# Optimization experiments

Measured on AMD Instinct MI355X. Metric: run time of the kernel, lower is better.

## Reference

```python
import jax, jax.numpy as jnp
import numpy as np

N_CELL, N_NET, N_GCELL = 50000, 10000, 20000
E = 100000
D = 32   # hidden_node = hidden_net = hidden_hanna = out_node = out_net
DP = 16  # hidden_pin = hidden_edge feats


def setup_inputs() -> dict:
    key = jax.random.key(0)
    ks = jax.random.split(key, 21)
    f = jax.random.normal
    ri = lambda k, n: jax.random.randint(k, (E,), 0, n, dtype=jnp.int32)
    return {
        'node_feat': f(ks[0], (N_CELL, D), jnp.float32),
        'net_feat': f(ks[1], (N_NET, D), jnp.float32),
        'pin_feat': f(ks[2], (E, DP), jnp.float32),
        'hanna_feat': f(ks[3], (N_GCELL, D), jnp.float32),
        'edge_feat': f(ks[4], (E, DP), jnp.float32),
        'pins_src': ri(ks[5], N_CELL), 'pins_dst': ri(ks[6], N_NET),
        'pinned_src': ri(ks[7], N_NET), 'pinned_dst': ri(ks[8], N_CELL),
        'connect_src': ri(ks[9], N_GCELL), 'connect_dst': ri(ks[10], N_GCELL),
        'pt_src': ri(ks[11], N_CELL), 'pt_dst': ri(ks[12], N_GCELL),
        'pf_src': ri(ks[13], N_GCELL), 'pf_dst': ri(ks[14], N_CELL),
        'W_net': f(ks[15], (D, D)) * 0.1, 'b_net': jnp.zeros((D,), jnp.float32),
        'W_topo': f(ks[16], (DP, D * D)) * 0.1, 'b_topo': jnp.zeros((D * D,), jnp.float32),
        'W_pins': f(ks[17], (D, D)) * 0.1, 'b_pins': jnp.zeros((D,), jnp.float32),
        'W_connect': f(ks[18], (D, D)) * 0.1, 'b_connect': jnp.zeros((D,), jnp.float32),
        'W_pt': f(ks[19], (D, D)) * 0.1, 'b_pt': jnp.zeros((D,), jnp.float32),
        'b_pinned': jnp.zeros((D,), jnp.float32), 'b_pf': jnp.zeros((D,), jnp.float32),
    }


def _deg(idx, n):
    # clamped degree, as DGL clamps to min 1
    return jnp.maximum(jax.ops.segment_sum(jnp.ones_like(idx, jnp.float32), idx, n), 1.0)


def graph_conv(h_src, W, b, src, dst, n_src, n_dst):
    # DGL GraphConv with norm='both': D_out^{-1/2} gather -> sum -> D_in^{-1/2}, then W, b
    feat = (h_src * _deg(src, n_src)[:, None] ** -0.5) @ W
    agg = jax.ops.segment_sum(feat[src], dst, n_dst)
    return agg * _deg(dst, n_dst)[:, None] ** -0.5 + b


def nn_conv(h_src, efeat, W_topo, b_topo, bias, src, dst, n_dst):
    # DGL NNConv (aggregator='mean'): per-edge weight from edge_func, mean over in-edges
    d_in = h_src.shape[1]
    w = (efeat @ W_topo + b_topo).reshape(-1, d_in, bias.shape[0])  # (E, d_in, d_out)
    m = jnp.einsum('ei,eio->eo', h_src[src], w)
    return jax.ops.segment_sum(m, dst, n_dst) / _deg(dst, n_dst)[:, None] + bias


def reference(node_feat, net_feat, pin_feat, hanna_feat, edge_feat,
              pins_src, pins_dst, pinned_src, pinned_dst, connect_src, connect_dst,
              pt_src, pt_dst, pf_src, pf_dst,
              W_net, b_net, W_topo, b_topo, W_pins, b_pins,
              W_connect, b_connect, W_pt, b_pt, b_pinned, b_pf):
    # 'pins': cell -> net (GraphConv)
    h_net = graph_conv(node_feat, W_pins, b_pins, pins_src, pins_dst, N_CELL, N_NET)
    # 'pinned': net -> cell (NNConv) + 'point-from': gcell -> cell (NNConv); agg='sum'
    h_cell = (nn_conv(net_feat, pin_feat, W_topo, b_topo, b_pinned, pinned_src, pinned_dst, N_CELL)
              + nn_conv(hanna_feat, edge_feat, W_topo, b_topo, b_pf, pf_src, pf_dst, N_CELL))
    # 'connect': gcell -> gcell + 'point-to': cell -> gcell (GraphConvs); agg='sum'
    h_gcell = (graph_conv(hanna_feat, W_connect, b_connect, connect_src, connect_dst, N_GCELL, N_GCELL)
               + graph_conv(node_feat, W_pt, b_pt, pt_src, pt_dst, N_CELL, N_GCELL))
    return (h_cell, h_net + net_feat @ W_net + b_net, h_gcell)
```

## Files before the change

### kernel.cpp

```cpp
#include <hip/hip_runtime.h>

typedef unsigned short u16;
typedef unsigned int u32;

#define NC 50000
#define NN 10000
#define NG 20000
#define NE 100000
#define NSCAN 150016
#define NBLK 74


__device__ __forceinline__ float bflo(u32 a) { return __uint_as_float(a << 16); }
__device__ __forceinline__ float bfhi(u32 a) { return __uint_as_float(a & 0xFFFF0000u); }
__device__ __forceinline__ u16 fbf(float f) {
  u32 u = __float_as_uint(f);
  return (u16)((u + 0x7FFFu + ((u >> 16) & 1u)) >> 16);
}

__device__ __forceinline__ float nn_msg(int e, int s, const float* __restrict__ ef,
                                        const u16* __restrict__ T,
                                        const float* __restrict__ C, int o) {
  const float4* efp = reinterpret_cast<const float4*>(ef + (size_t)e * 16);
  float4 ea = efp[0], eb = efp[1], ec = efp[2], ed = efp[3];
  const uint4* tp = reinterpret_cast<const uint4*>(T + (size_t)s * 512 + o * 16);
  uint4 ta = tp[0], tb = tp[1];
  float m = C[(size_t)s * 32 + o];
  m += ea.x * bflo(ta.x) + ea.y * bfhi(ta.x) + ea.z * bflo(ta.y) + ea.w * bfhi(ta.y);
  m += eb.x * bflo(ta.z) + eb.y * bfhi(ta.z) + eb.z * bflo(ta.w) + eb.w * bfhi(ta.w);
  m += ec.x * bflo(tb.x) + ec.y * bfhi(tb.x) + ec.z * bflo(tb.y) + ec.w * bfhi(tb.y);
  m += ed.x * bflo(tb.z) + ed.y * bfhi(tb.z) + ed.z * bflo(tb.w) + ed.w * bfhi(tb.w);
  return m;
}

__global__ __launch_bounds__(512) void k_front(
    const float* __restrict__ feat_net, const float* __restrict__ feat_han,
    const float* __restrict__ W_topo, const float* __restrict__ b_topo,
    u16* __restrict__ T_net, u16* __restrict__ T_han,
    float* __restrict__ C_net, float* __restrict__ C_han,
    const int* __restrict__ pins_src, const int* __restrict__ pins_dst,
    const int* __restrict__ pinned_dst, const int* __restrict__ pf_dst,
    const int* __restrict__ connect_src, const int* __restrict__ connect_dst,
    const int* __restrict__ pt_src, const int* __restrict__ pt_dst,
    int* __restrict__ hist, int* __restrict__ srccnt) {
  int b = blockIdx.x;
  int tid = threadIdx.x;
  if (b < 469) {
    __shared__ float hs[64][32];
    int nd0 = b * 64;
    {
      int idx = tid * 4;
      int nl = idx >> 5, i = idx & 31;
      int ng = min(nd0 + nl, 29999);
      const float* rp = (ng < NN) ? feat_net + (size_t)ng * 32
                                  : feat_han + (size_t)(ng - NN) * 32;
      *reinterpret_cast<float4*>(&hs[nl][i]) =
          *reinterpret_cast<const float4*>(rp + i);
    }
    int jj = tid & 127, grp = tid >> 7;
    int j0 = jj * 4;
    int o = j0 >> 4, p0 = j0 & 15;
    float w0[32], w1[32], w2[32], w3[32];
#pragma unroll
    for (int i = 0; i < 32; i++) {
      w0[i] = W_topo[(p0 + 0) * 1024 + i * 32 + o];
      w1[i] = W_topo[(p0 + 1) * 1024 + i * 32 + o];
      w2[i] = W_topo[(p0 + 2) * 1024 + i * 32 + o];
      w3[i] = W_topo[(p0 + 3) * 1024 + i * 32 + o];
    }
    __syncthreads();
#pragma unroll 2
    for (int n = 0; n < 16; n++) {
      int nl = grp * 16 + n;
      float a0 = 0.f, a1 = 0.f, a2 = 0.f, a3 = 0.f;
#pragma unroll
      for (int i4 = 0; i4 < 32; i4 += 4) {
        float4 h = *reinterpret_cast<float4*>(&hs[nl][i4]);
        a0 += h.x * w0[i4] + h.y * w0[i4 + 1] + h.z * w0[i4 + 2] + h.w * w0[i4 + 3];
        a1 += h.x * w1[i4] + h.y * w1[i4 + 1] + h.z * w1[i4 + 2] + h.w * w1[i4 + 3];
        a2 += h.x * w2[i4] + h.y * w2[i4 + 1] + h.z * w2[i4 + 2] + h.w * w2[i4 + 3];
        a3 += h.x * w3[i4] + h.y * w3[i4 + 1] + h.z * w3[i4 + 2] + h.w * w3[i4 + 3];
      }
      int s = nd0 + nl;
      if (s < 30000) {
        uint2 pk = make_uint2((u32)fbf(a0) | ((u32)fbf(a1) << 16),
                              (u32)fbf(a2) | ((u32)fbf(a3) << 16));
        u16* tb = (s < NN) ? T_net + (size_t)s * 512 + j0
                           : T_han + (size_t)(s - NN) * 512 + j0;
        *reinterpret_cast<uint2*>(tb) = pk;
      }
    }
    return;
  }
  if (b < 2344) {
    int t = (b - 469) * 512 + tid;
    int s2 = t >> 5, o = t & 31;
    bool han = s2 >= NN;
    const float* feat = han ? feat_han : feat_net;
    float* C = han ? C_han : C_net;
    int s = han ? s2 - NN : s2;
    float acc = 0.f;
#pragma unroll 8
    for (int i = 0; i < 32; i++)
      acc += feat[(size_t)s * 32 + i] * b_topo[i * 32 + o];
    C[(size_t)s * 32 + o] = acc;
    return;
  }
  int e = (b - 2344) * 512 + tid;
  if (e >= NE) return;
  atomicAdd(&hist[pins_dst[e]], 1);
  atomicAdd(&hist[10000 + connect_dst[e]], 1);
  atomicAdd(&hist[30000 + pt_dst[e]], 1);
  atomicAdd(&hist[50000 + pinned_dst[e]], 1);
  atomicAdd(&hist[100000 + pf_dst[e]], 1);
  atomicAdd(&srccnt[pins_src[e]], 1);
  atomicAdd(&srccnt[50000 + connect_src[e]], 1);
  atomicAdd(&srccnt[70000 + pt_src[e]], 1);
}

__global__ __launch_bounds__(256) void k_scan(
    const int* __restrict__ cnt, int* __restrict__ bases) {
  __shared__ int sm[256];
  __shared__ int carryS;
  int b = blockIdx.x, tid = threadIdx.x;
  int lim = b * 2048;
  int part = 0;
  for (int i = tid * 4; i < lim; i += 1024) {
    int4 v = *reinterpret_cast<const int4*>(cnt + i);
    part += v.x + v.y + v.z + v.w;
  }
  sm[tid] = part;
  __syncthreads();
  for (int off = 128; off > 0; off >>= 1) {
    if (tid < off) sm[tid] += sm[tid + off];
    __syncthreads();
  }
  if (tid == 0) carryS = sm[0];
  __syncthreads();
  int base = b * 2048 + tid * 8;
  int v[8];
  int tot = 0;
#pragma unroll
  for (int j = 0; j < 8; j++) {
    int i = base + j;
    v[j] = (i < NSCAN) ? cnt[i] : 0;
    tot += v[j];
  }
  sm[tid] = tot;
  __syncthreads();
  for (int off = 1; off < 256; off <<= 1) {
    int add = (tid >= off) ? sm[tid - off] : 0;
    __syncthreads();
    sm[tid] += add;
    __syncthreads();
  }
  int excl = sm[tid] - tot + carryS;
#pragma unroll
  for (int j = 0; j < 8; j++) {
    int i = base + j;
    if (i < NSCAN) bases[i] = excl;
    excl += v[j];
  }
}

__global__ __launch_bounds__(512) void k_fill(
    const int* __restrict__ pins_src, const int* __restrict__ pins_dst,
    const int* __restrict__ connect_src, const int* __restrict__ connect_dst,
    const int* __restrict__ pt_src, const int* __restrict__ pt_dst,
    const int* __restrict__ pinned_src, const int* __restrict__ pinned_dst,
    const int* __restrict__ pf_src, const int* __restrict__ pf_dst,
    const int* __restrict__ srccnt,
    const int* __restrict__ bases, int* __restrict__ cursor,
    int2* __restrict__ csr_gc, int2* __restrict__ csr_nn) {
  int t = blockIdx.x * 512 + threadIdx.x;
  if (t >= 5 * NE) return;
  int r = (t >= NE) + (t >= 2 * NE) + (t >= 3 * NE) + (t >= 4 * NE);
  int e = t - r * NE;
  const int* srcs = r == 0 ? pins_src : r == 1 ? connect_src
                   : r == 2 ? pt_src : r == 3 ? pinned_src : pf_src;
  const int* dsts = r == 0 ? pins_dst : r == 1 ? connect_dst
                   : r == 2 ? pt_dst : r == 3 ? pinned_dst : pf_dst;
  int off = r == 0 ? 0 : r == 1 ? 10000 : r == 2 ? 30000 : r == 3 ? 50000 : 100000;
  int s = srcs[e];
  int g = off + dsts[e];
  int pos = atomicAdd(&cursor[g], 1);
  int cpos = bases[g] + pos;
  if (r < 3) {
    int soff = r == 0 ? 0 : r == 1 ? 50000 : 70000;
    float w = rsqrtf(fmaxf((float)srccnt[soff + s], 1.f));
    csr_gc[cpos] = make_int2(s, __float_as_int(w));
  } else {
    csr_nn[cpos - 300000] = make_int2(e, s);
  }
}

__global__ __launch_bounds__(512) void k_gc_fin(
    const int* __restrict__ hist, const int* __restrict__ bases,
    const int2* __restrict__ csr_gc,
    const float* __restrict__ node_feat, const float* __restrict__ hanna_feat,
    const float* __restrict__ net_feat,
    const float* __restrict__ W_pins, const float* __restrict__ b_pins,
    const float* __restrict__ W_net, const float* __restrict__ b_net,
    const float* __restrict__ W_connect, const float* __restrict__ b_connect,
    const float* __restrict__ W_pt, const float* __restrict__ b_pt,
    float* __restrict__ out) {
  __shared__ float Wa[1024], Wb[1024];
  __shared__ float srow[16][32];
  int b = blockIdx.x, tid = threadIdx.x;
  if (b < 625) {
    for (int k = tid; k < 1024; k += 512) {
      Wa[k] = W_pins[k];
      Wb[k] = W_net[k];
    }
    int rl = tid >> 5, o = tid & 31;
    int r = b * 16 + rl;
    int base = bases[r], deg = hist[r];
    float acc = 0.f;
    int k = 0;
    for (; k + 1 < deg; k += 2) {
      int2 pa = csr_gc[base + k], pb = csr_gc[base + k + 1];
      acc += node_feat[(size_t)pa.x * 32 + o] * __int_as_float(pa.y) +
             node_feat[(size_t)pb.x * 32 + o] * __int_as_float(pb.y);
    }
    if (k < deg) {
      int2 pa = csr_gc[base + k];
      acc += node_feat[(size_t)pa.x * 32 + o] * __int_as_float(pa.y);
    }
    srow[rl][o] = acc;
    __syncthreads();
    float a1 = 0.f, a2 = 0.f;
#pragma unroll 8
    for (int i = 0; i < 32; i++) {
      a1 += srow[rl][i] * Wa[i * 32 + o];
      a2 += net_feat[(size_t)r * 32 + i] * Wb[i * 32 + o];
    }
    out[1600000 + (size_t)r * 32 + o] =
        a1 * rsqrtf(fmaxf((float)deg, 1.f)) + b_pins[o] + a2 + b_net[o];
    return;
  }
  int bb = b - 625;
  for (int k = tid; k < 1024; k += 512) {
    Wa[k] = W_connect[k];
    Wb[k] = W_pt[k];
  }
  int rl = tid >> 6;
  int half = (tid >> 5) & 1;
  int o = tid & 31;
  int r = bb * 8 + rl;
  int g = (half ? 30000 : 10000) + r;
  const float* feat = half ? node_feat : hanna_feat;
  int base = bases[g], deg = hist[g];
  float acc = 0.f;
  int k = 0;
  for (; k + 1 < deg; k += 2) {
    int2 pa = csr_gc[base + k], pb = csr_gc[base + k + 1];
    acc += feat[(size_t)pa.x * 32 + o] * __int_as_float(pa.y) +
           feat[(size_t)pb.x * 32 + o] * __int_as_float(pb.y);
  }
  if (k < deg) {
    int2 pa = csr_gc[base + k];
    acc += feat[(size_t)pa.x * 32 + o] * __int_as_float(pa.y);
  }
  srow[rl * 2 + half][o] = acc;
  __syncthreads();
  if (half == 0) {
    float a1 = 0.f, a2 = 0.f;
#pragma unroll 8
    for (int i = 0; i < 32; i++) {
      a1 += srow[rl * 2 + 0][i] * Wa[i * 32 + o];
      a2 += srow[rl * 2 + 1][i] * Wb[i * 32 + o];
    }
    out[1920000 + (size_t)r * 32 + o] =
        a1 * rsqrtf(fmaxf((float)hist[10000 + r], 1.f)) + b_connect[o] +
        a2 * rsqrtf(fmaxf((float)hist[30000 + r], 1.f)) + b_pt[o];
  }
}

__global__ __launch_bounds__(512) void k_tail(
    const int* __restrict__ hist, const int* __restrict__ bases,
    const int2* __restrict__ csr_nn,
    const float* __restrict__ pin_feat, const float* __restrict__ edge_feat,
    const u16* __restrict__ T_net, const u16* __restrict__ T_han,
    const float* __restrict__ C_net, const float* __restrict__ C_han,
    const float* __restrict__ b_pinned, const float* __restrict__ b_pf,
    float* __restrict__ out) {
  int t = blockIdx.x * 512 + threadIdx.x;
  int d = t >> 5, o = t & 31;
  float a0 = 0.f, a1 = 0.f;
  {
    int g = 50000 + d;
    int base = bases[g] - 300000, deg = hist[g];
    int k = 0;
    for (; k + 1 < deg; k += 2) {
      int2 ea = csr_nn[base + k], eb = csr_nn[base + k + 1];
      a0 += nn_msg(ea.x, ea.y, pin_feat, T_net, C_net, o) +
            nn_msg(eb.x, eb.y, pin_feat, T_net, C_net, o);
    }
    if (k < deg) {
      int2 ea = csr_nn[base + k];
      a0 += nn_msg(ea.x, ea.y, pin_feat, T_net, C_net, o);
    }
    a0 /= fmaxf((float)deg, 1.f);
  }
  {
    int g = 100000 + d;
    int base = bases[g] - 300000, deg = hist[g];
    int k = 0;
    for (; k + 1 < deg; k += 2) {
      int2 ea = csr_nn[base + k], eb = csr_nn[base + k + 1];
      a1 += nn_msg(ea.x, ea.y, edge_feat, T_han, C_han, o) +
            nn_msg(eb.x, eb.y, edge_feat, T_han, C_han, o);
    }
    if (k < deg) {
      int2 ea = csr_nn[base + k];
      a1 += nn_msg(ea.x, ea.y, edge_feat, T_han, C_han, o);
    }
    a1 /= fmaxf((float)deg, 1.f);
  }
  out[(size_t)d * 32 + o] = a0 + a1 + b_pinned[o] + b_pf[o];
}

extern "C" void kernel_launch(void* const* d_in, const int* in_sizes, int n_in,
                              void* d_out, int out_size, void* d_ws, size_t ws_size,
                              hipStream_t stream) {
  const float* node_feat  = (const float*)d_in[0];
  const float* net_feat   = (const float*)d_in[1];
  const float* pin_feat   = (const float*)d_in[2];
  const float* hanna_feat = (const float*)d_in[3];
  const float* edge_feat  = (const float*)d_in[4];
  const int* pins_src    = (const int*)d_in[5];
  const int* pins_dst    = (const int*)d_in[6];
  const int* pinned_src  = (const int*)d_in[7];
  const int* pinned_dst  = (const int*)d_in[8];
  const int* connect_src = (const int*)d_in[9];
  const int* connect_dst = (const int*)d_in[10];
  const int* pt_src      = (const int*)d_in[11];
  const int* pt_dst      = (const int*)d_in[12];
  const int* pf_src      = (const int*)d_in[13];
  const int* pf_dst      = (const int*)d_in[14];
  const float* W_net     = (const float*)d_in[15];
  const float* b_net     = (const float*)d_in[16];
  const float* W_topo    = (const float*)d_in[17];
  const float* b_topo    = (const float*)d_in[18];
  const float* W_pins    = (const float*)d_in[19];
  const float* b_pins    = (const float*)d_in[20];
  const float* W_connect = (const float*)d_in[21];
  const float* b_connect = (const float*)d_in[22];
  const float* W_pt      = (const float*)d_in[23];
  const float* b_pt      = (const float*)d_in[24];
  const float* b_pinned  = (const float*)d_in[25];
  const float* b_pf      = (const float*)d_in[26];
  float* out = (float*)d_out;

  int* wi = (int*)d_ws;
  int* hist    = wi + 0;
  int* cursor  = wi + 150016;
  int* srccnt  = wi + 300032;
  int* bases   = wi + 420032;
  int2* csr_gc = (int2*)(wi + 570192);
  int2* csr_nn = (int2*)(wi + 1170192);
  float* wf = (float*)d_ws;
  float* C_net  = wf + 1570192;
  float* C_han  = wf + 1890192;
  u16* T_net = (u16*)((char*)d_ws + 10120832);
  u16* T_han = (u16*)((char*)d_ws + 10120832 + 10240000);

  hipMemsetAsync(d_ws, 0, 420032 * sizeof(int), stream);

  k_front<<<2540, 512, 0, stream>>>(
      net_feat, hanna_feat, W_topo, b_topo, T_net, T_han, C_net, C_han,
      pins_src, pins_dst, pinned_dst, pf_dst, connect_src, connect_dst,
      pt_src, pt_dst, hist, srccnt);

  k_scan<<<NBLK, 256, 0, stream>>>(hist, bases);

  k_fill<<<(5 * NE + 511) / 512, 512, 0, stream>>>(
      pins_src, pins_dst, connect_src, connect_dst, pt_src, pt_dst,
      pinned_src, pinned_dst, pf_src, pf_dst, srccnt, bases, cursor,
      csr_gc, csr_nn);

  k_gc_fin<<<3125, 512, 0, stream>>>(
      hist, bases, csr_gc, node_feat, hanna_feat, net_feat,
      W_pins, b_pins, W_net, b_net, W_connect, b_connect, W_pt, b_pt, out);

  k_tail<<<3125, 512, 0, stream>>>(
      hist, bases, csr_nn, pin_feat, edge_feat,
      T_net, T_han, C_net, C_han, b_pinned, b_pf, out);
}
```

Before: 311.4 us.

## Retile W_topo transform via LDS, init cursor in scan, fuse tail into gc kernel

The per-node W_topo transform in k_front is retiled. Each block now stages half of the transposed W_topo slice in shared memory and computes 2 nodes × 8 outputs per thread, with 16-byte stores, replacing the per-thread 128-register weight arrays. The scan kernel now writes the cursor array with the exclusive bases, so k_fill no longer reads bases and the memset is smaller. The NNConv tail kernel is merged into the GraphConv finish kernel as one launch, which removes a launch boundary and lets the two independent workloads overlap, at the cost of higher LDS and register pressure in the combined kernel.

After: 457.8 us. 47.0% more time.

```diff
diff --git a/kernel.cpp b/kernel.cpp
--- a/kernel.cpp
+++ b/kernel.cpp
@@ -43,12 +43,17 @@
     const int* __restrict__ connect_src, const int* __restrict__ connect_dst,
     const int* __restrict__ pt_src, const int* __restrict__ pt_dst,
     int* __restrict__ hist, int* __restrict__ srccnt) {
+  __shared__ float hs[32][32];
+  __shared__ float wl[32 * 256];
   int b = blockIdx.x;
   int tid = threadIdx.x;
-  if (b < 469) {
-    __shared__ float hs[64][32];
-    int nd0 = b * 64;
-    {
+  if (b < 1876) {
+    int ntile = b >> 1;
+    int jhalf = b & 1;
+    int jbase = jhalf * 256;
+    int obase = jhalf * 16;
+    int nd0 = ntile * 32;
+    if (tid < 256) {
       int idx = tid * 4;
       int nl = idx >> 5, i = idx & 31;
       int ng = min(nd0 + nl, 29999);
@@ -57,43 +62,70 @@
       *reinterpret_cast<float4*>(&hs[nl][i]) =
           *reinterpret_cast<const float4*>(rp + i);
     }
-    int jj = tid & 127, grp = tid >> 7;
-    int j0 = jj * 4;
-    int o = j0 >> 4, p0 = j0 & 15;
-    float w0[32], w1[32], w2[32], w3[32];
+    for (int g = tid; g < 8192; g += 512) {
+      int p = g >> 9;
+      int i = (g >> 4) & 31;
+      int op = g & 15;
+      wl[i * 256 + op * 16 + p] = W_topo[p * 1024 + i * 32 + (obase + op)];
+    }
+    __syncthreads();
+    int jg = tid & 31, ng2 = tid >> 5;
+    int j0 = jg * 8;
+    int n0 = ng2 * 2;
+    float a0[8], a1[8];
 #pragma unroll
-    for (int i = 0; i < 32; i++) {
-      w0[i] = W_topo[(p0 + 0) * 1024 + i * 32 + o];
-      w1[i] = W_topo[(p0 + 1) * 1024 + i * 32 + o];
-      w2[i] = W_topo[(p0 + 2) * 1024 + i * 32 + o];
-      w3[i] = W_topo[(p0 + 3) * 1024 + i * 32 + o];
-    }
-    __syncthreads();
-#pragma unroll 2
-    for (int n = 0; n < 16; n++) {
-      int nl = grp * 16 + n;
-      float a0 = 0.f, a1 = 0.f, a2 = 0.f, a3 = 0.f;
+    for (int k = 0; k < 8; k++) { a0[k] = 0.f; a1[k] = 0.f; }
 #pragma unroll
-      for (int i4 = 0; i4 < 32; i4 += 4) {
-        float4 h = *reinterpret_cast<float4*>(&hs[nl][i4]);
-        a0 += h.x * w0[i4] + h.y * w0[i4 + 1] + h.z * w0[i4 + 2] + h.w * w0[i4 + 3];
-        a1 += h.x * w1[i4] + h.y * w1[i4 + 1] + h.z * w1[i4 + 2] + h.w * w1[i4 + 3];
-        a2 += h.x * w2[i4] + h.y * w2[i4 + 1] + h.z * w2[i4 + 2] + h.w * w2[i4 + 3];
-        a3 += h.x * w3[i4] + h.y * w3[i4 + 1] + h.z * w3[i4 + 2] + h.w * w3[i4 + 3];
-      }
-      int s = nd0 + nl;
-      if (s < 30000) {
-        uint2 pk = make_uint2((u32)fbf(a0) | ((u32)fbf(a1) << 16),
-                              (u32)fbf(a2) | ((u32)fbf(a3) << 16));
-        u16* tb = (s < NN) ? T_net + (size_t)s * 512 + j0
-                           : T_han + (size_t)(s - NN) * 512 + j0;
-        *reinterpret_cast<uint2*>(tb) = pk;
-      }
+    for (int i = 0; i < 32; i += 2) {
+      float2 ha = *reinterpret_cast<float2*>(&hs[n0][i]);
+      float2 hb = *reinterpret_cast<float2*>(&hs[n0 + 1][i]);
+      float4 w0a = *reinterpret_cast<float4*>(&wl[i * 256 + j0]);
+      float4 w0b = *reinterpret_cast<float4*>(&wl[i * 256 + j0 + 4]);
+      float4 w1a = *reinterpret_cast<float4*>(&wl[(i + 1) * 256 + j0]);
+      float4 w1b = *reinterpret_cast<float4*>(&wl[(i + 1) * 256 + j0 + 4]);
+      a0[0] += ha.x * w0a.x + ha.y * w1a.x;
+      a0[1] += ha.x * w0a.y + ha.y * w1a.y;
+      a0[2] += ha.x * w0a.z + ha.y * w1a.z;
+      a0[3] += ha.x * w0a.w + ha.y * w1a.w;
+      a0[4] += ha.x * w0b.x + ha.y * w1b.x;
+      a0[5] += ha.x * w0b.y + ha.y * w1b.y;
+      a0[6] += ha.x * w0b.z + ha.y * w1b.z;
+      a0[7] += ha.x * w0b.w + ha.y * w1b.w;
+      a1[0] += hb.x * w0a.x + hb.y * w1a.x;
+      a1[1] += hb.x * w0a.y + hb.y * w1a.y;
+      a1[2] += hb.x * w0a.z + hb.y * w1a.z;
+      a1[3] += hb.x * w0a.w + hb.y * w1a.w;
+      a1[4] += hb.x * w0b.x + hb.y * w1b.x;
+      a1[5] += hb.x * w0b.y + hb.y * w1b.y;
+      a1[6] += hb.x * w0b.z + hb.y * w1b.z;
+      a1[7] += hb.x * w0b.w + hb.y * w1b.w;
+    }
+    int s0 = nd0 + n0;
+    if (s0 < 30000) {
+      uint4 pk;
+      pk.x = (u32)fbf(a0[0]) | ((u32)fbf(a0[1]) << 16);
+      pk.y = (u32)fbf(a0[2]) | ((u32)fbf(a0[3]) << 16);
+      pk.z = (u32)fbf(a0[4]) | ((u32)fbf(a0[5]) << 16);
+      pk.w = (u32)fbf(a0[6]) | ((u32)fbf(a0[7]) << 16);
+      u16* tp = (s0 < NN ? T_net + (size_t)s0 * 512
+                         : T_han + (size_t)(s0 - NN) * 512) + jbase + j0;
+      *reinterpret_cast<uint4*>(tp) = pk;
+    }
+    int s1 = s0 + 1;
+    if (s1 < 30000) {
+      uint4 pk;
+      pk.x = (u32)fbf(a1[0]) | ((u32)fbf(a1[1]) << 16);
+      pk.y = (u32)fbf(a1[2]) | ((u32)fbf(a1[3]) << 16);
+      pk.z = (u32)fbf(a1[4]) | ((u32)fbf(a1[5]) << 16);
+      pk.w = (u32)fbf(a1[6]) | ((u32)fbf(a1[7]) << 16);
+      u16* tp = (s1 < NN ? T_net + (size_t)s1 * 512
+                         : T_han + (size_t)(s1 - NN) * 512) + jbase + j0;
+      *reinterpret_cast<uint4*>(tp) = pk;
     }
     return;
   }
-  if (b < 2344) {
-    int t = (b - 469) * 512 + tid;
+  if (b < 3751) {
+    int t = (b - 1876) * 512 + tid;
     int s2 = t >> 5, o = t & 31;
     bool han = s2 >= NN;
     const float* feat = han ? feat_han : feat_net;
@@ -106,7 +138,7 @@
     C[(size_t)s * 32 + o] = acc;
     return;
   }
-  int e = (b - 2344) * 512 + tid;
+  int e = (b - 3751) * 512 + tid;
   if (e >= NE) return;
   atomicAdd(&hist[pins_dst[e]], 1);
   atomicAdd(&hist[10000 + connect_dst[e]], 1);
@@ -119,7 +151,8 @@
 }
 
 __global__ __launch_bounds__(256) void k_scan(
-    const int* __restrict__ cnt, int* __restrict__ bases) {
+    const int* __restrict__ cnt, int* __restrict__ bases,
+    int* __restrict__ cursor) {
   __shared__ int sm[256];
   __shared__ int carryS;
   int b = blockIdx.x, tid = threadIdx.x;
@@ -158,7 +191,7 @@
 #pragma unroll
   for (int j = 0; j < 8; j++) {
     int i = base + j;
-    if (i < NSCAN) bases[i] = excl;
+    if (i < NSCAN) { bases[i] = excl; cursor[i] = excl; }
     excl += v[j];
   }
 }
@@ -169,8 +202,7 @@
     const int* __restrict__ pt_src, const int* __restrict__ pt_dst,
     const int* __restrict__ pinned_src, const int* __restrict__ pinned_dst,
     const int* __restrict__ pf_src, const int* __restrict__ pf_dst,
-    const int* __restrict__ srccnt,
-    const int* __restrict__ bases, int* __restrict__ cursor,
+    const int* __restrict__ srccnt, int* __restrict__ cursor,
     int2* __restrict__ csr_gc, int2* __restrict__ csr_nn) {
   int t = blockIdx.x * 512 + threadIdx.x;
   if (t >= 5 * NE) return;
@@ -184,21 +216,24 @@
   int s = srcs[e];
   int g = off + dsts[e];
   int pos = atomicAdd(&cursor[g], 1);
-  int cpos = bases[g] + pos;
   if (r < 3) {
     int soff = r == 0 ? 0 : r == 1 ? 50000 : 70000;
     float w = rsqrtf(fmaxf((float)srccnt[soff + s], 1.f));
-    csr_gc[cpos] = make_int2(s, __float_as_int(w));
+    csr_gc[pos] = make_int2(s, __float_as_int(w));
   } else {
-    csr_nn[cpos - 300000] = make_int2(e, s);
-  }
-}
-
-__global__ __launch_bounds__(512) void k_gc_fin(
+    csr_nn[pos - 300000] = make_int2(e, s);
+  }
+}
+
+__global__ __launch_bounds__(512) void k_big(
     const int* __restrict__ hist, const int* __restrict__ bases,
-    const int2* __restrict__ csr_gc,
+    const int2* __restrict__ csr_gc, const int2* __restrict__ csr_nn,
     const float* __restrict__ node_feat, const float* __restrict__ hanna_feat,
     const float* __restrict__ net_feat,
+    const float* __restrict__ pin_feat, const float* __restrict__ edge_feat,
+    const u16* __restrict__ T_net, const u16* __restrict__ T_han,
+    const float* __restrict__ C_net, const float* __restrict__ C_han,
+    const float* __restrict__ b_pinned, const float* __restrict__ b_pf,
     const float* __restrict__ W_pins, const float* __restrict__ b_pins,
     const float* __restrict__ W_net, const float* __restrict__ b_net,
     const float* __restrict__ W_connect, const float* __restrict__ b_connect,
@@ -207,13 +242,51 @@
   __shared__ float Wa[1024], Wb[1024];
   __shared__ float srow[16][32];
   int b = blockIdx.x, tid = threadIdx.x;
-  if (b < 625) {
+  if (b < 3125) {
+    int t = b * 512 + tid;
+    int d = t >> 5, o = t & 31;
+    float a0 = 0.f, a1 = 0.f;
+    {
+      int g = 50000 + d;
+      int base = bases[g] - 300000, deg = hist[g];
+      int k = 0;
+      for (; k + 1 < deg; k += 2) {
+        int2 ea = csr_nn[base + k], eb = csr_nn[base + k + 1];
+        a0 += nn_msg(ea.x, ea.y, pin_feat, T_net, C_net, o) +
+              nn_msg(eb.x, eb.y, pin_feat, T_net, C_net, o);
+      }
+      if (k < deg) {
+        int2 ea = csr_nn[base + k];
+        a0 += nn_msg(ea.x, ea.y, pin_feat, T_net, C_net, o);
+      }
+      a0 /= fmaxf((float)deg, 1.f);
+    }
+    {
+      int g = 100000 + d;
+      int base = bases[g] - 300000, deg = hist[g];
+      int k = 0;
+      for (; k + 1 < deg; k += 2) {
+        int2 ea = csr_nn[base + k], eb = csr_nn[base + k + 1];
+        a1 += nn_msg(ea.x, ea.y, edge_feat, T_han, C_han, o) +
+              nn_msg(eb.x, eb.y, edge_feat, T_han, C_han, o);
+      }
+      if (k < deg) {
+        int2 ea = csr_nn[base + k];
+        a1 += nn_msg(ea.x, ea.y, edge_feat, T_han, C_han, o);
+      }
+      a1 /= fmaxf((float)deg, 1.f);
+    }
+    out[(size_t)d * 32 + o] = a0 + a1 + b_pinned[o] + b_pf[o];
+    return;
+  }
+  if (b < 3750) {
+    int bb = b - 3125;
     for (int k = tid; k < 1024; k += 512) {
       Wa[k] = W_pins[k];
       Wb[k] = W_net[k];
     }
     int rl = tid >> 5, o = tid & 31;
-    int r = b * 16 + rl;
+    int r = bb * 16 + rl;
     int base = bases[r], deg = hist[r];
     float acc = 0.f;
     int k = 0;
@@ -238,7 +311,7 @@
         a1 * rsqrtf(fmaxf((float)deg, 1.f)) + b_pins[o] + a2 + b_net[o];
     return;
   }
-  int bb = b - 625;
+  int bb = b - 3750;
   for (int k = tid; k < 1024; k += 512) {
     Wa[k] = W_connect[k];
     Wb[k] = W_pt[k];
@@ -274,50 +347,6 @@
         a1 * rsqrtf(fmaxf((float)hist[10000 + r], 1.f)) + b_connect[o] +
         a2 * rsqrtf(fmaxf((float)hist[30000 + r], 1.f)) + b_pt[o];
   }
-}
-
-__global__ __launch_bounds__(512) void k_tail(
-    const int* __restrict__ hist, const int* __restrict__ bases,
-    const int2* __restrict__ csr_nn,
-    const float* __restrict__ pin_feat, const float* __restrict__ edge_feat,
-    const u16* __restrict__ T_net, const u16* __restrict__ T_han,
-    const float* __restrict__ C_net, const float* __restrict__ C_han,
-    const float* __restrict__ b_pinned, const float* __restrict__ b_pf,
-    float* __restrict__ out) {
-  int t = blockIdx.x * 512 + threadIdx.x;
-  int d = t >> 5, o = t & 31;
-  float a0 = 0.f, a1 = 0.f;
-  {
-    int g = 50000 + d;
-    int base = bases[g] - 300000, deg = hist[g];
-    int k = 0;
-    for (; k + 1 < deg; k += 2) {
-      int2 ea = csr_nn[base + k], eb = csr_nn[base + k + 1];
-      a0 += nn_msg(ea.x, ea.y, pin_feat, T_net, C_net, o) +
-            nn_msg(eb.x, eb.y, pin_feat, T_net, C_net, o);
-    }
-    if (k < deg) {
-      int2 ea = csr_nn[base + k];
-      a0 += nn_msg(ea.x, ea.y, pin_feat, T_net, C_net, o);
-    }
-    a0 /= fmaxf((float)deg, 1.f);
-  }
-  {
-    int g = 100000 + d;
-    int base = bases[g] - 300000, deg = hist[g];
-    int k = 0;
-    for (; k + 1 < deg; k += 2) {
-      int2 ea = csr_nn[base + k], eb = csr_nn[base + k + 1];
-      a1 += nn_msg(ea.x, ea.y, edge_feat, T_han, C_han, o) +
-            nn_msg(eb.x, eb.y, edge_feat, T_han, C_han, o);
-    }
-    if (k < deg) {
-      int2 ea = csr_nn[base + k];
-      a1 += nn_msg(ea.x, ea.y, edge_feat, T_han, C_han, o);
-    }
-    a1 /= fmaxf((float)deg, 1.f);
-  }
-  out[(size_t)d * 32 + o] = a0 + a1 + b_pinned[o] + b_pf[o];
 }
 
 extern "C" void kernel_launch(void* const* d_in, const int* in_sizes, int n_in,
@@ -354,36 +383,33 @@
 
   int* wi = (int*)d_ws;
   int* hist    = wi + 0;
-  int* cursor  = wi + 150016;
-  int* srccnt  = wi + 300032;
-  int* bases   = wi + 420032;
-  int2* csr_gc = (int2*)(wi + 570192);
-  int2* csr_nn = (int2*)(wi + 1170192);
+  int* srccnt  = wi + 150016;
+  int* bases   = wi + 270032;
+  int* cursor  = wi + 420048;
+  int2* csr_gc = (int2*)(wi + 570064);
+  int2* csr_nn = (int2*)(wi + 1170064);
   float* wf = (float*)d_ws;
-  float* C_net  = wf + 1570192;
-  float* C_han  = wf + 1890192;
-  u16* T_net = (u16*)((char*)d_ws + 10120832);
-  u16* T_han = (u16*)((char*)d_ws + 10120832 + 10240000);
-
-  hipMemsetAsync(d_ws, 0, 420032 * sizeof(int), stream);
-
-  k_front<<<2540, 512, 0, stream>>>(
+  float* C_net  = wf + 1570064;
+  float* C_han  = wf + 1890064;
+  u16* T_net = (u16*)((char*)d_ws + 10120256);
+  u16* T_han = (u16*)((char*)d_ws + 10120256 + 10240000);
+
+  hipMemsetAsync(d_ws, 0, 270032 * sizeof(int), stream);
+
+  k_front<<<3947, 512, 0, stream>>>(
       net_feat, hanna_feat, W_topo, b_topo, T_net, T_han, C_net, C_han,
       pins_src, pins_dst, pinned_dst, pf_dst, connect_src, connect_dst,
       pt_src, pt_dst, hist, srccnt);
 
-  k_scan<<<NBLK, 256, 0, stream>>>(hist, bases);
+  k_scan<<<NBLK, 256, 0, stream>>>(hist, bases, cursor);
 
   k_fill<<<(5 * NE + 511) / 512, 512, 0, stream>>>(
       pins_src, pins_dst, connect_src, connect_dst, pt_src, pt_dst,
-      pinned_src, pinned_dst, pf_src, pf_dst, srccnt, bases, cursor,
+      pinned_src, pinned_dst, pf_src, pf_dst, srccnt, cursor,
       csr_gc, csr_nn);
 
-  k_gc_fin<<<3125, 512, 0, stream>>>(
-      hist, bases, csr_gc, node_feat, hanna_feat, net_feat,
+  k_big<<<6250, 512, 0, stream>>>(
+      hist, bases, csr_gc, csr_nn, node_feat, hanna_feat, net_feat,
+      pin_feat, edge_feat, T_net, T_han, C_net, C_han, b_pinned, b_pf,
       W_pins, b_pins, W_net, b_net, W_connect, b_connect, W_pt, b_pt, out);
-
-  k_tail<<<3125, 512, 0, stream>>>(
-      hist, bases, csr_nn, pin_feat, edge_feat,
-      T_net, T_han, C_net, C_han, b_pinned, b_pf, out);
-}
+}
```
